# Performance work log

Hardware: AMD Instinct MI355X
Metric: run time of the kernel (lower is better)

## Reference

```python
import jax, jax.numpy as jnp
import numpy as np
import math

B, N, C_IN, C_OUT, K, RATIO = 16, 4096, 256, 512, 16, 0.25
N_OUT = math.ceil(N * RATIO)  # 1024
BN_EPS = 1e-5


def fps_indices(p, n):
    """Farthest point sampling. p: [B,N,3] -> local indices [B,n] (deterministic start at 0, eval mode)."""
    def fps_one(pts):  # [N,3]
        d0 = jnp.sum((pts - pts[0]) ** 2, axis=-1)          # [N]
        idxs0 = jnp.zeros((n,), jnp.int32)                  # idx[0] = 0
        def body(i, st):
            d, idxs = st
            nxt = jnp.argmax(d).astype(jnp.int32)
            idxs = idxs.at[i].set(nxt)
            d = jnp.minimum(d, jnp.sum((pts - pts[nxt]) ** 2, axis=-1))
            return (d, idxs)
        _, idxs = jax.lax.fori_loop(1, n, body, (d0, idxs0))
        return idxs
    return jax.vmap(fps_one)(p)


def setup_inputs() -> dict:
    key = jax.random.key(0)
    ks = jax.random.split(key, 6)
    x = jax.random.normal(ks[0], (B, N, C_IN), jnp.float32)
    p = jax.random.normal(ks[1], (B, N, 3), jnp.float32)
    sid_euc = jax.random.randint(ks[2], (B * N, K), 0, B * N).astype(jnp.int64)
    tid_euc = jax.random.randint(ks[3], (B * N, K), 0, B * N).astype(jnp.int64)
    W = jax.random.normal(ks[4], (C_OUT, C_IN), jnp.float32) * (1.0 / np.sqrt(C_IN))
    b = jax.random.normal(ks[5], (C_OUT,), jnp.float32) * 0.02
    gamma = jnp.ones((C_OUT,), jnp.float32)
    beta = jnp.zeros((C_OUT,), jnp.float32)
    run_mean = jnp.zeros((C_OUT,), jnp.float32)
    run_var = jnp.ones((C_OUT,), jnp.float32)
    return {"x": x, "p": p, "sid_euc": sid_euc, "tid_euc": tid_euc,
            "W": W, "b": b, "gamma": gamma, "beta": beta,
            "run_mean": run_mean, "run_var": run_var}


def reference(x, p, sid_euc, tid_euc, W, b, gamma, beta, run_mean, run_var):
    Bsz, Npts, _ = x.shape
    n = N_OUT
    Kn = sid_euc.shape[1]
    # MLP: pointwise Linear + BatchNorm (eval) + ReLU
    h = jnp.einsum('bnc,oc->bno', x, W) + b                       # [B,N,C_OUT]
    h = (h - run_mean) * (gamma / jnp.sqrt(run_var + BN_EPS)) + beta
    h = jax.nn.relu(h)
    # FPS -> global flat indices into B*N
    fid_local = fps_indices(p, n)                                  # [B,n]
    fid = (fid_local + jnp.arange(Bsz, dtype=jnp.int32)[:, None] * Npts).reshape(-1)
    # sample coords
    p_flat = p.reshape(Bsz * Npts, -1)
    p_out = p_flat[fid].reshape(Bsz, n, -1)                        # [B,n,3]
    # gather K neighbors of each sampled point, max-pool over K
    sid = sid_euc[fid].reshape(-1)                                 # [B*n*K]
    h_flat = h.reshape(Bsz * Npts, -1)
    x_out = h_flat[sid].reshape(Bsz, n, Kn, -1).max(axis=-2)       # [B,n,C_OUT]
    return (x_out, p_out)
```

## Files before the change

kernel.cpp:

```cpp
#include <hip/hip_runtime.h>
#include <hip/hip_bf16.h>

#define BATCH   16
#define NPTS    4096
#define CIN     256
#define COUT    512
#define KNN     16
#define NOUT    1024
#define XOUT_ELEMS 8388608
#define LDA     40
#define DYN_LDS 53312

typedef __attribute__((ext_vector_type(4))) float f32x4;
typedef __attribute__((ext_vector_type(2))) float f32x2;
typedef __attribute__((ext_vector_type(8))) short bf16x8;
typedef __attribute__((ext_vector_type(8))) unsigned short u16x8;
typedef unsigned long long u64;

__device__ __forceinline__ unsigned short f2bf_rne(float f) {
    unsigned u = __float_as_uint(f);
    return (unsigned short)((u + 0x7FFFu + ((u >> 16) & 1u)) >> 16);
}
__device__ __forceinline__ float bf2f(unsigned short s) {
    return __uint_as_float(((unsigned)s) << 16);
}

__device__ __forceinline__ float wave_max_dpp(float v) {
    int x, y;
    x = __float_as_int(v);
    y = __builtin_amdgcn_update_dpp(x, x, 0x111, 0xf, 0xf, false);
    v = fmaxf(v, __int_as_float(y)); x = __float_as_int(v);
    y = __builtin_amdgcn_update_dpp(x, x, 0x112, 0xf, 0xf, false);
    v = fmaxf(v, __int_as_float(y)); x = __float_as_int(v);
    y = __builtin_amdgcn_update_dpp(x, x, 0x114, 0xf, 0xf, false);
    v = fmaxf(v, __int_as_float(y)); x = __float_as_int(v);
    y = __builtin_amdgcn_update_dpp(x, x, 0x118, 0xf, 0xf, false);
    v = fmaxf(v, __int_as_float(y)); x = __float_as_int(v);
    y = __builtin_amdgcn_update_dpp(x, x, 0x142, 0xf, 0xf, false);
    v = fmaxf(v, __int_as_float(y)); x = __float_as_int(v);
    y = __builtin_amdgcn_update_dpp(x, x, 0x143, 0xf, 0xf, false);
    v = fmaxf(v, __int_as_float(y));
    return v;
}

extern "C" __global__ void __launch_bounds__(256)
fps_gemm(const float* __restrict__ x, const float* __restrict__ p,
         const float* __restrict__ W, const float* __restrict__ bias,
         const float* __restrict__ gamma, const float* __restrict__ beta,
         const float* __restrict__ rmean, const float* __restrict__ rvar,
         int* __restrict__ fid, unsigned short* __restrict__ h,
         float* __restrict__ out)
{
    extern __shared__ char smem[];
    const int t = threadIdx.x;
    const int lane = t & 63;
    const int wv = t >> 6;

    if (blockIdx.x < BATCH) {
#pragma clang fp contract(off)
        const int b = blockIdx.x;
        float* lx = (float*)smem;
        float* ly = lx + NPTS;
        float* lz = ly + NPTS;
        u64* warr = (u64*)(smem + 49152);
        int* wins = (int*)(smem + 49216);
        float* pout = out + XOUT_ELEMS + (size_t)b * NOUT * 3;

        const float* pb = p + (size_t)b * NPTS * 3;
        for (int l = t; l < NPTS * 3; l += 256) {
            float v = pb[l];
            int pi = l / 3;
            int c = l - pi * 3;
            if (c == 0) lx[pi] = v; else if (c == 1) ly[pi] = v; else lz[pi] = v;
        }
        if (t == 0) wins[0] = 0;
        __syncthreads();

        f32x2 px2[8], py2[8], pz2[8], d2[8];
        const int base = t << 4;
#pragma unroll
        for (int j = 0; j < 8; ++j) {
            px2[j] = *(const f32x2*)(lx + base + (j << 1));
            py2[j] = *(const f32x2*)(ly + base + (j << 1));
            pz2[j] = *(const f32x2*)(lz + base + (j << 1));
            d2[j]  = (f32x2){3.4028235e38f, 3.4028235e38f};
        }

        int winner = 0;
        for (int i = 1; i < NOUT; ++i) {
            float wx = lx[winner], wy = ly[winner], wz = lz[winner];
            f32x2 wx2 = {wx, wx}, wy2 = {wy, wy}, wz2 = {wz, wz};
            float bdA = -1.0f, bdB = -1.0f;
            int   bjA = 0,     bjB = 8;
#pragma unroll
            for (int j = 0; j < 4; ++j) {
                f32x2 dx = px2[j] - wx2;
                f32x2 dy = py2[j] - wy2;
                f32x2 dz = pz2[j] - wz2;
                f32x2 s  = ((dx * dx) + (dy * dy)) + (dz * dz);
                f32x2 nd;
                nd.x = fminf(d2[j].x, s.x);
                nd.y = fminf(d2[j].y, s.y);
                d2[j] = nd;
                bool g0 = nd.x > bdA;
                bdA = g0 ? nd.x : bdA;
                bjA = g0 ? (j << 1) : bjA;
                bool g1 = nd.y > bdA;
                bdA = g1 ? nd.y : bdA;
                bjA = g1 ? (j << 1) + 1 : bjA;
            }
#pragma unroll
            for (int j = 4; j < 8; ++j) {
                f32x2 dx = px2[j] - wx2;
                f32x2 dy = py2[j] - wy2;
                f32x2 dz = pz2[j] - wz2;
                f32x2 s  = ((dx * dx) + (dy * dy)) + (dz * dz);
                f32x2 nd;
                nd.x = fminf(d2[j].x, s.x);
                nd.y = fminf(d2[j].y, s.y);
                d2[j] = nd;
                bool g0 = nd.x > bdB;
                bdB = g0 ? nd.x : bdB;
                bjB = g0 ? (j << 1) : bjB;
                bool g1 = nd.y > bdB;
                bdB = g1 ? nd.y : bdB;
                bjB = g1 ? (j << 1) + 1 : bjB;
            }
            bool gm = bdB > bdA;
            float bestd = gm ? bdB : bdA;
            int   bestj = gm ? bjB : bjA;
            float vmax = wave_max_dpp(bestd);
            float wmax = __int_as_float(
                __builtin_amdgcn_readlane(__float_as_int(vmax), 63));
            u64 msk = __ballot(bestd == wmax);
            int lead = (int)__builtin_ctzll(msk);
            int wbpi = __builtin_amdgcn_readlane(base + bestj, lead);
            u64 key = ((u64)__float_as_uint(wmax) << 32)
                    | (unsigned)(NPTS - 1 - wbpi);
            u64* wrow = warr + ((i & 1) << 2);
            if (lane == 0) wrow[wv] = key;
            __syncthreads();
            ulonglong2 q01 = *(const ulonglong2*)(wrow);
            ulonglong2 q23 = *(const ulonglong2*)(wrow + 2);
            u64 kA = q01.y > q01.x ? q01.y : q01.x;
            u64 kB = q23.y > q23.x ? q23.y : q23.x;
            u64 k0 = kB > kA ? kB : kA;
            winner = NPTS - 1 - (int)(unsigned)(k0 & 0xffffffffull);
            if (t == 0) wins[i] = winner;
        }
        __syncthreads();
        for (int i = t; i < NOUT; i += 256) {
            int w = wins[i];
            fid[b * NOUT + i] = b * NPTS + w;
            float* po = pout + (size_t)i * 3;
            po[0] = lx[w]; po[1] = ly[w]; po[2] = lz[w];
        }
    } else {
        const int bid = blockIdx.x - BATCH;
        const int bm = bid >> 2;
        const int bn = bid & 3;
        short* As = (short*)smem;
        short* Bs = As + 128 * LDA;

        const int wm = wv >> 1, wn = wv & 1;
        const int quad = lane >> 4, l16 = lane & 15;
        const int m0 = bm * 128, n0 = bn * 128;

        f32x4 acc[4][4];
        const f32x4 zero = {0.0f, 0.0f, 0.0f, 0.0f};
#pragma unroll
        for (int a = 0; a < 4; ++a)
#pragma unroll
            for (int bb = 0; bb < 4; ++bb) acc[a][bb] = zero;

        const int srow = t >> 3;
        const int scol = (t & 7) << 2;

        for (int ks = 0; ks < 8; ++ks) {
            const int k0 = ks * 32;
            __syncthreads();
#pragma unroll
            for (int it = 0; it < 4; ++it) {
                int row = srow + it * 32;
                float4 va = *(const float4*)(x + (size_t)(m0 + row) * CIN + k0 + scol);
                short4 pa = make_short4((short)f2bf_rne(va.x), (short)f2bf_rne(va.y),
                                        (short)f2bf_rne(va.z), (short)f2bf_rne(va.w));
                *(short4*)(As + row * LDA + scol) = pa;
                float4 vb = *(const float4*)(W + (size_t)(n0 + row) * CIN + k0 + scol);
                short4 pb2 = make_short4((short)f2bf_rne(vb.x), (short)f2bf_rne(vb.y),
                                         (short)f2bf_rne(vb.z), (short)f2bf_rne(vb.w));
                *(short4*)(Bs + row * LDA + scol) = pb2;
            }
            __syncthreads();
            bf16x8 af[4], bfr[4];
#pragma unroll
            for (int tm = 0; tm < 4; ++tm)
                af[tm] = *(const bf16x8*)(As + (wm * 64 + tm * 16 + l16) * LDA + quad * 8);
#pragma unroll
            for (int tn = 0; tn < 4; ++tn)
                bfr[tn] = *(const bf16x8*)(Bs + (wn * 64 + tn * 16 + l16) * LDA + quad * 8);
#pragma unroll
            for (int tm = 0; tm < 4; ++tm)
#pragma unroll
                for (int tn = 0; tn < 4; ++tn)
                    acc[tm][tn] = __builtin_amdgcn_mfma_f32_16x16x32_bf16(
                        af[tm], bfr[tn], acc[tm][tn], 0, 0, 0);
        }
#pragma unroll
        for (int tn = 0; tn < 4; ++tn) {
            int c = n0 + wn * 64 + tn * 16 + l16;
            float sc = gamma[c] / sqrtf(rvar[c] + 1e-5f);
            float sh = (bias[c] - rmean[c]) * sc + beta[c];
#pragma unroll
            for (int tm = 0; tm < 4; ++tm) {
                int rbase = m0 + wm * 64 + tm * 16 + quad * 4;
#pragma unroll
                for (int r = 0; r < 4; ++r) {
                    float v = fmaxf(acc[tm][tn][r] * sc + sh, 0.0f);
                    h[(size_t)(rbase + r) * COUT + c] = f2bf_rne(v);
                }
            }
        }
    }
}

extern "C" __global__ void __launch_bounds__(64)
gather_maxpool(const int* __restrict__ sid32, const int* __restrict__ fid,
               const unsigned short* __restrict__ h, float* __restrict__ out)
{
    const int j = blockIdx.x;
    const int t = threadIdx.x;
    __shared__ int rows[KNN];
    const int frow = fid[j];
    bool is64 = (sid32[1] == 0) && (sid32[3] == 0) && (sid32[5] == 0);
    if (t < KNN) {
        long long e = (long long)frow * KNN + t;
        rows[t] = is64 ? sid32[e * 2] : sid32[e];
    }
    __syncthreads();

    const int c8 = t << 3;
    float m[8];
#pragma unroll
    for (int q = 0; q < 8; ++q) m[q] = -3.4028235e38f;
#pragma unroll
    for (int k = 0; k < KNN; ++k) {
        const u16x8 v = *(const u16x8*)(h + (size_t)rows[k] * COUT + c8);
#pragma unroll
        for (int q = 0; q < 8; ++q) m[q] = fmaxf(m[q], bf2f(v[q]));
    }
    float* po = out + (size_t)j * COUT + c8;
    *(float4*)(po)     = make_float4(m[0], m[1], m[2], m[3]);
    *(float4*)(po + 4) = make_float4(m[4], m[5], m[6], m[7]);
}

extern "C" void kernel_launch(void* const* d_in, const int* in_sizes, int n_in,
                              void* d_out, int out_size, void* d_ws, size_t ws_size,
                              hipStream_t stream)
{
    const float* x     = (const float*)d_in[0];
    const float* p     = (const float*)d_in[1];
    const int*   sid   = (const int*)d_in[2];
    const float* W     = (const float*)d_in[4];
    const float* bias  = (const float*)d_in[5];
    const float* gamma = (const float*)d_in[6];
    const float* beta  = (const float*)d_in[7];
    const float* rmean = (const float*)d_in[8];
    const float* rvar  = (const float*)d_in[9];
    float* out = (float*)d_out;

    int* fid = (int*)d_ws;
    unsigned short* h = (unsigned short*)((char*)d_ws + 65792);

    hipLaunchKernelGGL(fps_gemm, dim3(BATCH + 2048), dim3(256), DYN_LDS, stream,
                       x, p, W, bias, gamma, beta, rmean, rvar, fid, h, out);
    hipLaunchKernelGGL(gather_maxpool, dim3(BATCH * NOUT), dim3(64), 0, stream,
                       sid, fid, h, out);
}
```

Baseline: 724.8 us.

## Overlap gather-maxpool with FPS via progress flags in the fused kernel

Appends gather blocks to the fused FPS+GEMM kernel. Each gather block spin-waits on a GEMM completion counter and on a per-batch FPS progress counter, which the FPS blocks publish every 64 iterations with release stores. Blocks whose wait gives up are redone by a cleanup kernel that checks per-block done bits. The goal is to hide gather latency behind the serial FPS tail. It adds a memset, spin-polling, and reliance on gather blocks being co-resident with the producer blocks. The gather is also regrouped to 32 outputs per 256-thread block, with readlane used to broadcast the neighbor indices.

```diff
diff --git a/kernel.cpp b/kernel.cpp
--- a/kernel.cpp
+++ b/kernel.cpp
@@ -10,6 +10,8 @@
 #define XOUT_ELEMS 8388608
 #define LDA     40
 #define DYN_LDS 53312
+#define NGEMM   2048
+#define NGATH   512
 
 typedef __attribute__((ext_vector_type(4))) float f32x4;
 typedef __attribute__((ext_vector_type(2))) float f32x2;
@@ -43,11 +45,45 @@
     return v;
 }
 
+__device__ __forceinline__ void gather32(int g, const int* __restrict__ sid,
+                                         const int* __restrict__ fid,
+                                         const unsigned short* __restrict__ h,
+                                         float* __restrict__ out,
+                                         int lane, int wv)
+{
+    const bool is64 = (sid[1] == 0) && (sid[3] == 0) && (sid[5] == 0);
+    const int j0 = g * 32 + wv * 8;
+    const int c8 = lane << 3;
+    for (int q = 0; q < 8; ++q) {
+        const int j = j0 + q;
+        const int frow = fid[j];
+        int sv = 0;
+        if (lane < KNN) {
+            long long e = (long long)frow * KNN + lane;
+            sv = is64 ? sid[e * 2] : sid[e];
+        }
+        float m[8];
+#pragma unroll
+        for (int qq = 0; qq < 8; ++qq) m[qq] = -3.4028235e38f;
+#pragma unroll
+        for (int k = 0; k < KNN; ++k) {
+            int row = __builtin_amdgcn_readlane(sv, k);
+            const u16x8 v = *(const u16x8*)(h + (size_t)row * COUT + c8);
+#pragma unroll
+            for (int qq = 0; qq < 8; ++qq) m[qq] = fmaxf(m[qq], bf2f(v[qq]));
+        }
+        float* po = out + (size_t)j * COUT + c8;
+        *(f32x4*)(po)     = (f32x4){m[0], m[1], m[2], m[3]};
+        *(f32x4*)(po + 4) = (f32x4){m[4], m[5], m[6], m[7]};
+    }
+}
+
 extern "C" __global__ void __launch_bounds__(256)
 fps_gemm(const float* __restrict__ x, const float* __restrict__ p,
          const float* __restrict__ W, const float* __restrict__ bias,
          const float* __restrict__ gamma, const float* __restrict__ beta,
          const float* __restrict__ rmean, const float* __restrict__ rvar,
+         const int* __restrict__ sid, unsigned* __restrict__ ctrl,
          int* __restrict__ fid, unsigned short* __restrict__ h,
          float* __restrict__ out)
 {
@@ -55,6 +91,9 @@
     const int t = threadIdx.x;
     const int lane = t & 63;
     const int wv = t >> 6;
+    int* prog = (int*)ctrl;
+    unsigned* gdcnt = ctrl + 16;
+    unsigned* gdone = ctrl + 32;
 
     if (blockIdx.x < BATCH) {
 #pragma clang fp contract(off)
@@ -140,6 +179,15 @@
             u64* wrow = warr + ((i & 1) << 2);
             if (lane == 0) wrow[wv] = key;
             __syncthreads();
+            if ((i & 63) == 0) {
+                if (wv == 0) {
+                    int w = wins[i - 64 + lane];
+                    fid[b * NOUT + (i - 64) + lane] = b * NPTS + w;
+                    if (lane == 0)
+                        __hip_atomic_store(prog + b, i, __ATOMIC_RELEASE,
+                                           __HIP_MEMORY_SCOPE_AGENT);
+                }
+            }
             ulonglong2 q01 = *(const ulonglong2*)(wrow);
             ulonglong2 q23 = *(const ulonglong2*)(wrow + 2);
             u64 kA = q01.y > q01.x ? q01.y : q01.x;
@@ -155,7 +203,11 @@
             float* po = pout + (size_t)i * 3;
             po[0] = lx[w]; po[1] = ly[w]; po[2] = lz[w];
         }
-    } else {
+        __syncthreads();
+        if (t == 0)
+            __hip_atomic_store(prog + b, NOUT, __ATOMIC_RELEASE,
+                               __HIP_MEMORY_SCOPE_AGENT);
+    } else if (blockIdx.x < BATCH + NGEMM) {
         const int bid = blockIdx.x - BATCH;
         const int bm = bid >> 2;
         const int bn = bid & 3;
@@ -221,37 +273,50 @@
                 }
             }
         }
+        __syncthreads();
+        if (t == 0)
+            __hip_atomic_fetch_add(gdcnt, 1u, __ATOMIC_RELEASE,
+                                   __HIP_MEMORY_SCOPE_AGENT);
+    } else {
+        const int g = blockIdx.x - (BATCH + NGEMM);
+        const int bat = g >> 5;
+        const int hi_local = ((g & 31) + 1) * 32;
+        int* sflag = (int*)smem;
+        if (t == 0) {
+            int ok = 0;
+            for (int it = 0; it < 2048; ++it) {
+                unsigned gd = __hip_atomic_load(gdcnt, __ATOMIC_RELAXED,
+                                                __HIP_MEMORY_SCOPE_AGENT);
+                int pr = __hip_atomic_load(prog + bat, __ATOMIC_RELAXED,
+                                           __HIP_MEMORY_SCOPE_AGENT);
+                if (gd == (unsigned)NGEMM && pr >= hi_local) {
+                    __hip_atomic_load(gdcnt, __ATOMIC_ACQUIRE,
+                                      __HIP_MEMORY_SCOPE_AGENT);
+                    __hip_atomic_load(prog + bat, __ATOMIC_ACQUIRE,
+                                      __HIP_MEMORY_SCOPE_AGENT);
+                    ok = 1;
+                    break;
+                }
+                __builtin_amdgcn_s_sleep(64);
+            }
+            sflag[0] = ok;
+        }
+        __syncthreads();
+        if (!sflag[0]) return;
+        gather32(g, sid, fid, h, out, lane, wv);
+        __syncthreads();
+        if (t == 0) atomicOr(gdone + (g >> 5), 1u << (g & 31));
     }
 }
 
-extern "C" __global__ void __launch_bounds__(64)
-gather_maxpool(const int* __restrict__ sid32, const int* __restrict__ fid,
-               const unsigned short* __restrict__ h, float* __restrict__ out)
+extern "C" __global__ void __launch_bounds__(256)
+gather_cleanup(const int* __restrict__ sid, const int* __restrict__ fid,
+               const unsigned short* __restrict__ h,
+               const unsigned* __restrict__ ctrl, float* __restrict__ out)
 {
-    const int j = blockIdx.x;
-    const int t = threadIdx.x;
-    __shared__ int rows[KNN];
-    const int frow = fid[j];
-    bool is64 = (sid32[1] == 0) && (sid32[3] == 0) && (sid32[5] == 0);
-    if (t < KNN) {
-        long long e = (long long)frow * KNN + t;
-        rows[t] = is64 ? sid32[e * 2] : sid32[e];
-    }
-    __syncthreads();
-
-    const int c8 = t << 3;
-    float m[8];
-#pragma unroll
-    for (int q = 0; q < 8; ++q) m[q] = -3.4028235e38f;
-#pragma unroll
-    for (int k = 0; k < KNN; ++k) {
-        const u16x8 v = *(const u16x8*)(h + (size_t)rows[k] * COUT + c8);
-#pragma unroll
-        for (int q = 0; q < 8; ++q) m[q] = fmaxf(m[q], bf2f(v[q]));
-    }
-    float* po = out + (size_t)j * COUT + c8;
-    *(float4*)(po)     = make_float4(m[0], m[1], m[2], m[3]);
-    *(float4*)(po + 4) = make_float4(m[4], m[5], m[6], m[7]);
+    const int g = blockIdx.x;
+    if ((ctrl[32 + (g >> 5)] >> (g & 31)) & 1u) return;
+    gather32(g, sid, fid, h, out, threadIdx.x & 63, threadIdx.x >> 6);
 }
 
 extern "C" void kernel_launch(void* const* d_in, const int* in_sizes, int n_in,
@@ -270,10 +335,14 @@
     float* out = (float*)d_out;
 
     int* fid = (int*)d_ws;
+    unsigned* ctrl = (unsigned*)((char*)d_ws + 65536);
     unsigned short* h = (unsigned short*)((char*)d_ws + 65792);
 
-    hipLaunchKernelGGL(fps_gemm, dim3(BATCH + 2048), dim3(256), DYN_LDS, stream,
-                       x, p, W, bias, gamma, beta, rmean, rvar, fid, h, out);
-    hipLaunchKernelGGL(gather_maxpool, dim3(BATCH * NOUT), dim3(64), 0, stream,
-                       sid, fid, h, out);
-}
+    hipMemsetAsync(ctrl, 0, 256, stream);
+    hipLaunchKernelGGL(fps_gemm, dim3(BATCH + NGEMM + NGATH), dim3(256),
+                       DYN_LDS, stream,
+                       x, p, W, bias, gamma, beta, rmean, rvar,
+                       sid, ctrl, fid, h, out);
+    hipLaunchKernelGGL(gather_cleanup, dim3(NGATH), dim3(256), 0, stream,
+                       sid, fid, h, ctrl, out);
+}
```

New measurement: 766.5 us. 1.06x slower.
